# Kernel optimization log

Hardware: AMD Instinct MI355X
Metric: run time of the kernel (lower is better)

The kernel has to match this reference:

```python
import jax, jax.numpy as jnp
import numpy as np

OUT, N_GROUPS, GROUP = 11008, 32, 128
IN = N_GROUPS * GROUP  # 4096
RANK = 128
B, S = 1, 64


def setup_inputs() -> dict:
    key = jax.random.key(0)
    ks = jax.random.split(key, 7)
    x = jax.random.normal(ks[0], (B, S, IN), dtype=jnp.float32)
    weight = jax.random.randint(ks[1], (OUT, N_GROUPS, GROUP), 0, 16, dtype=jnp.int32)
    scale = jax.random.uniform(ks[2], (OUT, N_GROUPS), dtype=jnp.float32) * 0.02 + 1e-3
    zero_point = jax.random.uniform(ks[3], (OUT, N_GROUPS), dtype=jnp.float32) * 15.0
    svd_up = jax.random.normal(ks[4], (OUT, RANK), dtype=jnp.float32) * 0.02
    svd_down = jax.random.normal(ks[5], (RANK, IN), dtype=jnp.float32) * 0.02
    bias = jax.random.normal(ks[6], (OUT,), dtype=jnp.float32) * 0.01
    return {"x": x, "weight": weight, "scale": scale, "zero_point": zero_point,
            "svd_up": svd_up, "svd_down": svd_down, "bias": bias}


def _dequantize(weight, scale, zero_point, svd_up, svd_down):
    # group-wise dequant: (W_q - zp) * scale, per (out, group) pair
    W = (weight.astype(jnp.float32) - zero_point[:, :, None]) * scale[:, :, None]
    W = W.reshape(weight.shape[0], -1)  # [OUT, IN]
    # low-rank SVD correction
    return W + svd_up @ svd_down


def reference(x, weight, scale, zero_point, svd_up, svd_down, bias):
    # int8 dynamic-quant path (token count 64 >= 16, int8_matmul=True)
    xt = x.reshape(-1, x.shape[-1])                       # [T, IN]
    W_f = _dequantize(weight, scale, zero_point, svd_up, svd_down).T  # [IN, OUT]
    scale_x = jnp.max(jnp.abs(xt), axis=1, keepdims=True) / 127.0     # [T, 1]
    x_q = jnp.clip(jnp.round(xt / scale_x), -128, 127).astype(jnp.int8)
    scale_w = jnp.max(jnp.abs(W_f), axis=0, keepdims=True) / 127.0    # [1, OUT]
    W_q8 = jnp.clip(jnp.round(W_f / scale_w), -128, 127).astype(jnp.int8)
    acc = jnp.matmul(x_q, W_q8, preferred_element_type=jnp.int32)     # [T, OUT] int32
    out = acc.astype(jnp.float32) * scale_x * scale_w
    return out[None] + bias  # [1, T, OUT], matching torch's unsqueeze(0) + bias
```

## Files before the change

kernel.cpp:

```cpp
#include <hip/hip_runtime.h>
#include <string.h>

#define OUT_DIM 11008
#define IN_DIM  4096
#define NTOK    64
#define RANK    128
#define NG      32

typedef float        v4f  __attribute__((ext_vector_type(4)));
typedef int          v4i  __attribute__((ext_vector_type(4)));
typedef unsigned int v4u  __attribute__((ext_vector_type(4)));
typedef unsigned int v2u  __attribute__((ext_vector_type(2)));
typedef _Float16     v8h  __attribute__((ext_vector_type(8)));

__device__ inline unsigned int pack2h(float lo, float hi) {
  union { _Float16 h[2]; unsigned int u; } t;
  t.h[0] = (_Float16)lo; t.h[1] = (_Float16)hi;
  return t.u;
}

__global__ __launch_bounds__(256) void pack_d_kernel(const float* __restrict__ d,
                                                     unsigned int* __restrict__ dp) {
  int idx = (blockIdx.x * 256 + threadIdx.x) * 4;
  int r2 = idx >> 12, c = idx & 4095;
  v4f a = *(const v4f*)(d + (2 * r2) * IN_DIM + c);
  v4f b = *(const v4f*)(d + (2 * r2 + 1) * IN_DIM + c);
  v4u o;
#pragma unroll
  for (int e = 0; e < 4; e++) o[e] = pack2h(a[e], b[e]);
  *(v4u*)(dp + idx) = o;
}

__device__ inline void load_u(const float* __restrict__ svd_up, _Float16 (*U)[136],
                              int tid, int r0) {
#pragma unroll
  for (int i = 0; i < 16; i++) {
    int idx = i * 256 + tid;
    int r = idx >> 7, k = idx & 127;
    U[r][k] = (_Float16)svd_up[(r0 + r) * RANK + k];
  }
}

__device__ inline void stage_d(const unsigned int* __restrict__ dp, unsigned int (*Dl)[128],
                               int tid, int kt) {
  int c = (tid & 31) * 4;
#pragma unroll
  for (int i = 0; i < 8; i++) {
    int r2 = i * 8 + (tid >> 5);
    *(v4u*)&Dl[r2][c] = *(const v4u*)(dp + r2 * IN_DIM + kt * 128 + c);
  }
}

__device__ inline void svd_mfma(const _Float16 (*U)[136], const unsigned int (*Dl)[128],
                                int l, int w, v4f acc[2][2]) {
#pragma unroll
  for (int ks = 0; ks < 4; ks++) {
    v8h a0 = *(const v8h*)&U[(l & 15)][ks * 32 + (l >> 4) * 8];
    v8h a1 = *(const v8h*)&U[16 + (l & 15)][ks * 32 + (l >> 4) * 8];
#pragma unroll
    for (int fn = 0; fn < 2; fn++) {
      int col = w * 32 + fn * 16 + (l & 15);
      int rb = ks * 16 + (l >> 4) * 4;
      union { unsigned int u[4]; v8h h; } bu;
      bu.u[0] = Dl[rb][col];
      bu.u[1] = Dl[rb + 1][col];
      bu.u[2] = Dl[rb + 2][col];
      bu.u[3] = Dl[rb + 3][col];
      acc[0][fn] = __builtin_amdgcn_mfma_f32_16x16x32_f16(a0, bu.h, acc[0][fn], 0, 0, 0);
      acc[1][fn] = __builtin_amdgcn_mfma_f32_16x16x32_f16(a1, bu.h, acc[1][fn], 0, 0, 0);
    }
  }
}

__global__ __launch_bounds__(256) void cgemm_kernel(const float* __restrict__ svd_up,
    const unsigned int* __restrict__ dp, _Float16* __restrict__ Cb) {
  __shared__ _Float16 U[32][136];
  __shared__ unsigned int Dl[64][128];
  int tid = threadIdx.x;
  int r0 = blockIdx.x * 32;
  load_u(svd_up, U, tid, r0);
  int l = tid & 63, w = tid >> 6;
  __syncthreads();
  for (int ct = 0; ct < 4; ct++) {
    int ktile = blockIdx.y * 4 + ct;
    stage_d(dp, Dl, tid, ktile);
    __syncthreads();
    v4f acc[2][2] = {};
    svd_mfma(U, Dl, l, w, acc);
#pragma unroll
    for (int fm = 0; fm < 2; fm++)
#pragma unroll
      for (int fn = 0; fn < 2; fn++)
#pragma unroll
        for (int j = 0; j < 4; j++) {
          int row = r0 + fm * 16 + (l >> 4) * 4 + j;
          int col = ktile * 128 + w * 32 + fn * 16 + (l & 15);
          Cb[row * IN_DIM + col] = (_Float16)acc[fm][fn][j];
        }
    __syncthreads();
  }
}

__global__ __launch_bounds__(256) void rowmax_kernel(const int* __restrict__ wq,
    const float* __restrict__ scale, const float* __restrict__ zp,
    const _Float16* __restrict__ Cb, unsigned int* __restrict__ wpk,
    float* __restrict__ swmax) {
  int tid = threadIdx.x;
  int lane = tid & 63, w = tid >> 6;
  int r = blockIdx.x * 4 + w;
  const int* wrow = wq + r * IN_DIM;
  const _Float16* crow = Cb + r * IN_DIM;
  unsigned int* prow = wpk + r * (IN_DIM / 8);
  const float* srow = scale + r * NG;
  const float* zrow = zp + r * NG;
  float m = 0.f;
  for (int j = 0; j < 8; j++) {
    int d = j * 64 + lane;
    int e0 = d * 8;
    v4i w0 = *(const v4i*)(wrow + e0);
    v4i w1 = *(const v4i*)(wrow + e0 + 4);
    union { v4u u; _Float16 h[8]; } cc;
    cc.u = *(const v4u*)(crow + e0);
    int g = e0 >> 7;
    float s = srow[g], z = zrow[g];
    unsigned int o = (unsigned)(w0[0] & 15)         | ((unsigned)(w0[1] & 15) << 4)
                   | ((unsigned)(w0[2] & 15) << 8)  | ((unsigned)(w0[3] & 15) << 12)
                   | ((unsigned)(w1[0] & 15) << 16) | ((unsigned)(w1[1] & 15) << 20)
                   | ((unsigned)(w1[2] & 15) << 24) | ((unsigned)(w1[3] & 15) << 28);
    prow[d] = o;
#pragma unroll
    for (int k = 0; k < 4; k++) {
      m = fmaxf(m, fabsf(((float)w0[k] - z) * s + (float)cc.h[k]));
      m = fmaxf(m, fabsf(((float)w1[k] - z) * s + (float)cc.h[k + 4]));
    }
  }
#pragma unroll
  for (int off = 1; off < 64; off <<= 1) m = fmaxf(m, __shfl_xor(m, off));
  if (lane == 0) swmax[r] = m;
}

__global__ __launch_bounds__(256) void quant_x_kernel(const float* __restrict__ x,
                                                      signed char* __restrict__ xq,
                                                      float* __restrict__ sx) {
  int t = blockIdx.x, tid = threadIdx.x;
  const float* row = x + t * IN_DIM;
  v4f v[4];
  float m = 0.f;
#pragma unroll
  for (int i = 0; i < 4; i++) {
    v[i] = *(const v4f*)(row + tid * 16 + i * 4);
#pragma unroll
    for (int e = 0; e < 4; e++) m = fmaxf(m, fabsf(v[i][e]));
  }
#pragma unroll
  for (int off = 1; off < 64; off <<= 1) m = fmaxf(m, __shfl_xor(m, off));
  __shared__ float wm[4];
  if ((tid & 63) == 0) wm[tid >> 6] = m;
  __syncthreads();
  m = fmaxf(fmaxf(wm[0], wm[1]), fmaxf(wm[2], wm[3]));
  float s = m / 127.0f;
  if (tid == 0) sx[t] = s;
  unsigned int packed[4];
#pragma unroll
  for (int i = 0; i < 4; i++) {
    int q[4];
#pragma unroll
    for (int e = 0; e < 4; e++) {
      float qf = rintf(v[i][e] / s);
      qf = fminf(127.f, fmaxf(-128.f, qf));
      q[e] = (int)qf;
    }
    packed[i] = (q[0] & 255) | ((q[1] & 255) << 8) | ((q[2] & 255) << 16) | ((q[3] & 255) << 24);
  }
  *(v4u*)(xq + t * IN_DIM + tid * 16) = *(v4u*)packed;
}

__global__ __launch_bounds__(256) void matmul_kernel(const unsigned int* __restrict__ wpk,
    const float* __restrict__ scale, const float* __restrict__ zp,
    const _Float16* __restrict__ Cb, const signed char* __restrict__ xq,
    const float* __restrict__ swmax, int* __restrict__ acc32) {
  __shared__ unsigned int W8[32][33];
  int tid = threadIdx.x;
  int r0 = blockIdx.x * 32;
  int kc = blockIdx.y;
  int l = tid & 63, w = tid >> 6;
  int myrow = tid >> 3, c0 = (tid & 7) * 16;
  float swr = swmax[r0 + myrow] / 127.0f;
  v4i oacc[2] = {};
  for (int kt = 0; kt < 8; kt++) {
    int kbase = kc * 1024 + kt * 128;
    int g = kbase >> 7;
    float s = scale[(r0 + myrow) * NG + g];
    float z = zp[(r0 + myrow) * NG + g];
    v2u pk = *(const v2u*)(wpk + (r0 + myrow) * (IN_DIM / 8) + ((kbase + c0) >> 3));
    union { v4u u[2]; _Float16 h[16]; } cc;
    cc.u[0] = *(const v4u*)(Cb + (r0 + myrow) * IN_DIM + kbase + c0);
    cc.u[1] = *(const v4u*)(Cb + (r0 + myrow) * IN_DIM + kbase + c0 + 8);
    unsigned int wd[4];
#pragma unroll
    for (int i = 0; i < 4; i++) {
      int q[4];
#pragma unroll
      for (int e = 0; e < 4; e++) {
        int jj = i * 4 + e;
        int qn = (pk[jj >> 3] >> (4 * (jj & 7))) & 15;
        float W = ((float)qn - z) * s + (float)cc.h[jj];
        float qf = rintf(W / swr);
        qf = fminf(127.f, fmaxf(-128.f, qf));
        q[e] = (int)qf;
      }
      wd[i] = (q[0] & 255) | ((q[1] & 255) << 8) | ((q[2] & 255) << 16) | ((q[3] & 255) << 24);
    }
    __syncthreads();
#pragma unroll
    for (int i = 0; i < 4; i++) W8[myrow][(c0 >> 2) + i] = wd[i];
    __syncthreads();
#pragma unroll
    for (int ks = 0; ks < 2; ks++) {
      v4i a = *(const v4i*)(xq + (w * 16 + (l & 15)) * IN_DIM + kbase + ks * 64 + (l >> 4) * 16);
#pragma unroll
      for (int fr = 0; fr < 2; fr++) {
        int rr = fr * 16 + (l & 15);
        int kd = ks * 16 + (l >> 4) * 4;
        v4i b;
        b[0] = (int)W8[rr][kd];
        b[1] = (int)W8[rr][kd + 1];
        b[2] = (int)W8[rr][kd + 2];
        b[3] = (int)W8[rr][kd + 3];
        oacc[fr] = __builtin_amdgcn_mfma_i32_16x16x64_i8(a, b, oacc[fr], 0, 0, 0);
      }
    }
  }
#pragma unroll
  for (int fr = 0; fr < 2; fr++)
#pragma unroll
    for (int j = 0; j < 4; j++) {
      int token = w * 16 + (l >> 4) * 4 + j;
      int orow = r0 + fr * 16 + (l & 15);
      atomicAdd(acc32 + token * OUT_DIM + orow, oacc[fr][j]);
    }
}

__global__ __launch_bounds__(256) void epilogue_kernel(const int* __restrict__ acc32,
    const float* __restrict__ sx, const float* __restrict__ swmax,
    const float* __restrict__ bias, float* __restrict__ out) {
  int o = blockIdx.x * 256 + threadIdx.x;
  int t = blockIdx.y;
  float swv = swmax[o] / 127.0f;
  out[t * OUT_DIM + o] = (float)acc32[t * OUT_DIM + o] * sx[t] * swv + bias[o];
}

extern "C" void kernel_launch(void* const* d_in, const int* in_sizes, int n_in,
                              void* d_out, int out_size, void* d_ws, size_t ws_size,
                              hipStream_t stream) {
  (void)in_sizes; (void)n_in; (void)out_size; (void)ws_size;
  const float* x        = (const float*)d_in[0];
  const int*   wq       = (const int*)d_in[1];
  const float* scale    = (const float*)d_in[2];
  const float* zp       = (const float*)d_in[3];
  const float* svd_up   = (const float*)d_in[4];
  const float* svd_down = (const float*)d_in[5];
  const float* bias     = (const float*)d_in[6];
  float* out = (float*)d_out;

  char* ws = (char*)d_ws;
  unsigned int* dp    = (unsigned int*)(ws);
  signed char*  xq    = (signed char*)(ws + 1048576);
  float*        sx    = (float*)(ws + 1310720);
  float*        swmax = (float*)(ws + 1310976);
  unsigned int* wpk   = (unsigned int*)(ws + 1355008);
  _Float16*     Cb    = (_Float16*)(ws + 23899392);
  int*          acc32 = (int*)(ws + 114076928);

  pack_d_kernel<<<256, 256, 0, stream>>>(svd_down, dp);
  cgemm_kernel<<<dim3(OUT_DIM / 32, 8), 256, 0, stream>>>(svd_up, dp, Cb);
  rowmax_kernel<<<OUT_DIM / 4, 256, 0, stream>>>(wq, scale, zp, Cb, wpk, swmax);
  quant_x_kernel<<<NTOK, 256, 0, stream>>>(x, xq, sx);
  hipMemsetAsync(acc32, 0, NTOK * OUT_DIM * sizeof(int), stream);
  matmul_kernel<<<dim3(OUT_DIM / 32, 4), 256, 0, stream>>>(wpk, scale, zp, Cb, xq, swmax, acc32);
  epilogue_kernel<<<dim3(OUT_DIM / 256, NTOK), 256, 0, stream>>>(acc32, sx, swmax, bias, out);
}
```

Measured before the change: 352.7 us.

## Coalesce Cb stores via LDS and replace atomics with split-K partial slabs

The cgemm kernel now stages its fp16 results in shared memory and writes them to global memory as 16-byte vector stores, instead of scattered 2-byte stores. The int8 matmul splits K into 8 chunks, and each chunk writes plain partial sums to its own slab; the epilogue adds up the slabs, so the atomics and the memset go away. This doubles matmul parallelism but makes the epilogue read extra partial buffers and enlarges the workspace footprint. It also launches quant_x earlier and unrolls the rowmax loop.

```diff
diff --git a/kernel.cpp b/kernel.cpp
--- a/kernel.cpp
+++ b/kernel.cpp
@@ -6,6 +6,7 @@
 #define NTOK    64
 #define RANK    128
 #define NG      32
+#define KSPLIT  8
 
 typedef float        v4f  __attribute__((ext_vector_type(4)));
 typedef int          v4i  __attribute__((ext_vector_type(4)));
@@ -76,10 +77,12 @@
     const unsigned int* __restrict__ dp, _Float16* __restrict__ Cb) {
   __shared__ _Float16 U[32][136];
   __shared__ unsigned int Dl[64][128];
+  __shared__ _Float16 Clh[32][136];
   int tid = threadIdx.x;
   int r0 = blockIdx.x * 32;
   load_u(svd_up, U, tid, r0);
   int l = tid & 63, w = tid >> 6;
+  int srow = tid >> 3, sc = (tid & 7) * 16;
   __syncthreads();
   for (int ct = 0; ct < 4; ct++) {
     int ktile = blockIdx.y * 4 + ct;
@@ -92,12 +95,12 @@
 #pragma unroll
       for (int fn = 0; fn < 2; fn++)
 #pragma unroll
-        for (int j = 0; j < 4; j++) {
-          int row = r0 + fm * 16 + (l >> 4) * 4 + j;
-          int col = ktile * 128 + w * 32 + fn * 16 + (l & 15);
-          Cb[row * IN_DIM + col] = (_Float16)acc[fm][fn][j];
-        }
-    __syncthreads();
+        for (int j = 0; j < 4; j++)
+          Clh[fm * 16 + (l >> 4) * 4 + j][w * 32 + fn * 16 + (l & 15)] = (_Float16)acc[fm][fn][j];
+    __syncthreads();
+    _Float16* dst = Cb + (r0 + srow) * IN_DIM + ktile * 128 + sc;
+    *(v4u*)dst       = *(const v4u*)&Clh[srow][sc];
+    *(v4u*)(dst + 8) = *(const v4u*)&Clh[srow][sc + 8];
   }
 }
 
@@ -114,6 +117,7 @@
   const float* srow = scale + r * NG;
   const float* zrow = zp + r * NG;
   float m = 0.f;
+#pragma unroll 4
   for (int j = 0; j < 8; j++) {
     int d = j * 64 + lane;
     int e0 = d * 8;
@@ -178,7 +182,7 @@
 __global__ __launch_bounds__(256) void matmul_kernel(const unsigned int* __restrict__ wpk,
     const float* __restrict__ scale, const float* __restrict__ zp,
     const _Float16* __restrict__ Cb, const signed char* __restrict__ xq,
-    const float* __restrict__ swmax, int* __restrict__ acc32) {
+    const float* __restrict__ swmax, int* __restrict__ pacc) {
   __shared__ unsigned int W8[32][33];
   int tid = threadIdx.x;
   int r0 = blockIdx.x * 32;
@@ -187,8 +191,8 @@
   int myrow = tid >> 3, c0 = (tid & 7) * 16;
   float swr = swmax[r0 + myrow] / 127.0f;
   v4i oacc[2] = {};
-  for (int kt = 0; kt < 8; kt++) {
-    int kbase = kc * 1024 + kt * 128;
+  for (int kt = 0; kt < 4; kt++) {
+    int kbase = kc * 512 + kt * 128;
     int g = kbase >> 7;
     float s = scale[(r0 + myrow) * NG + g];
     float z = zp[(r0 + myrow) * NG + g];
@@ -231,23 +235,28 @@
       }
     }
   }
+  int* slab = pacc + kc * (NTOK * OUT_DIM);
 #pragma unroll
   for (int fr = 0; fr < 2; fr++)
 #pragma unroll
     for (int j = 0; j < 4; j++) {
       int token = w * 16 + (l >> 4) * 4 + j;
       int orow = r0 + fr * 16 + (l & 15);
-      atomicAdd(acc32 + token * OUT_DIM + orow, oacc[fr][j]);
-    }
-}
-
-__global__ __launch_bounds__(256) void epilogue_kernel(const int* __restrict__ acc32,
+      slab[token * OUT_DIM + orow] = oacc[fr][j];
+    }
+}
+
+__global__ __launch_bounds__(256) void epilogue_kernel(const int* __restrict__ pacc,
     const float* __restrict__ sx, const float* __restrict__ swmax,
     const float* __restrict__ bias, float* __restrict__ out) {
   int o = blockIdx.x * 256 + threadIdx.x;
   int t = blockIdx.y;
+  int acc = 0;
+#pragma unroll
+  for (int kc = 0; kc < KSPLIT; kc++)
+    acc += pacc[kc * (NTOK * OUT_DIM) + t * OUT_DIM + o];
   float swv = swmax[o] / 127.0f;
-  out[t * OUT_DIM + o] = (float)acc32[t * OUT_DIM + o] * sx[t] * swv + bias[o];
+  out[t * OUT_DIM + o] = (float)acc * sx[t] * swv + bias[o];
 }
 
 extern "C" void kernel_launch(void* const* d_in, const int* in_sizes, int n_in,
@@ -270,13 +279,12 @@
   float*        swmax = (float*)(ws + 1310976);
   unsigned int* wpk   = (unsigned int*)(ws + 1355008);
   _Float16*     Cb    = (_Float16*)(ws + 23899392);
-  int*          acc32 = (int*)(ws + 114076928);
+  int*          pacc  = (int*)(ws + 114076928);
 
   pack_d_kernel<<<256, 256, 0, stream>>>(svd_down, dp);
+  quant_x_kernel<<<NTOK, 256, 0, stream>>>(x, xq, sx);
   cgemm_kernel<<<dim3(OUT_DIM / 32, 8), 256, 0, stream>>>(svd_up, dp, Cb);
   rowmax_kernel<<<OUT_DIM / 4, 256, 0, stream>>>(wq, scale, zp, Cb, wpk, swmax);
-  quant_x_kernel<<<NTOK, 256, 0, stream>>>(x, xq, sx);
-  hipMemsetAsync(acc32, 0, NTOK * OUT_DIM * sizeof(int), stream);
-  matmul_kernel<<<dim3(OUT_DIM / 32, 4), 256, 0, stream>>>(wpk, scale, zp, Cb, xq, swmax, acc32);
-  epilogue_kernel<<<dim3(OUT_DIM / 256, NTOK), 256, 0, stream>>>(acc32, sx, swmax, bias, out);
-}
+  matmul_kernel<<<dim3(OUT_DIM / 32, KSPLIT), 256, 0, stream>>>(wpk, scale, zp, Cb, xq, swmax, pacc);
+  epilogue_kernel<<<dim3(OUT_DIM / 256, NTOK), 256, 0, stream>>>(pacc, sx, swmax, bias, out);
+}
```

Result: no change. 353.3 us (+0.2%).
